# Kernel optimization log

Hardware: AMD Instinct MI355X
Metric: run time of the kernel (lower is better)

Reference implementation:

```python
import jax, jax.numpy as jnp
import numpy as np

E, N, D, H = 500000, 100000, 8, 256
BN_EPS = 1e-5


def _batchnorm(x, gamma, beta):
    # BatchNorm1d in training mode: biased batch statistics over dim 0
    mu = jnp.mean(x, axis=0)
    var = jnp.var(x, axis=0)
    return (x - mu) * jax.lax.rsqrt(var + BN_EPS) * gamma + beta


def _encoder(x, W1, b1, gamma, beta, W2, b2):
    h = jax.nn.relu(x @ W1 + b1)
    h = _batchnorm(h, gamma, beta)
    return h @ W2 + b2


def setup_inputs() -> dict:
    key = jax.random.key(0)
    ks = jax.random.split(key, 24)
    s = 0.05  # weight init scale
    inp = {
        "edge_attr": jax.random.normal(ks[0], (E, D), dtype=jnp.float32),
        "node_features": jax.random.normal(ks[1], (N, D), dtype=jnp.float32),
        "edge_index": jax.random.randint(ks[2], (2, E), 0, N, dtype=jnp.int32),
        "e_W1": jax.random.normal(ks[3], (D, H)) * s,
        "e_b1": jax.random.normal(ks[4], (H,)) * s,
        "e_gamma": jnp.ones((H,), jnp.float32),
        "e_beta": jnp.zeros((H,), jnp.float32),
        "e_W2": jax.random.normal(ks[5], (H, H)) * s,
        "e_b2": jax.random.normal(ks[6], (H,)) * s,
        "n_W1": jax.random.normal(ks[7], (D, H)) * s,
        "n_b1": jax.random.normal(ks[8], (H,)) * s,
        "n_gamma": jnp.ones((H,), jnp.float32),
        "n_beta": jnp.zeros((H,), jnp.float32),
        "n_W2": jax.random.normal(ks[9], (H, H)) * s,
        "n_b2": jax.random.normal(ks[10], (H,)) * s,
        "Wv": jax.random.normal(ks[11], (H, H)) * s,
        "bv": jax.random.normal(ks[12], (H,)) * s,
        "Wo": jax.random.normal(ks[13], (H, H)) * s,
        "bo": jax.random.normal(ks[14], (H,)) * s,
        "Wp": jax.random.normal(ks[15], (H, D)) * s,
        "bp": jax.random.normal(ks[16], (D,)) * s,
    }
    return inp


def reference(edge_attr, node_features, edge_index,
              e_W1, e_b1, e_gamma, e_beta, e_W2, e_b2,
              n_W1, n_b1, n_gamma, n_beta, n_W2, n_b2,
              Wv, bv, Wo, bo, Wp, bp):
    # edge encoder: Linear -> ReLU -> BatchNorm1d -> Linear
    edge_encoded = _encoder(edge_attr, e_W1, e_b1, e_gamma, e_beta, e_W2, e_b2)

    # gather endpoint features and average (node dim == edge dim, slice is no-op)
    src = node_features[edge_index[0]]  # [E, D]
    tgt = node_features[edge_index[1]]  # [E, D]
    node_context = (src + tgt) * 0.5
    node_encoded = _encoder(node_context, n_W1, n_b1, n_gamma, n_beta, n_W2, n_b2)

    # MultiheadAttention with seq_len=1: softmax over one key is exactly 1,
    # so output = out_proj(v_proj(node_encoded)); q/k projections cancel.
    attn_out = (node_encoded @ Wv + bv) @ Wo + bo  # [E, H]

    edge_attr_enhanced = attn_out @ Wp + bp  # [E, D]
    return edge_attr + 0.5 * edge_attr_enhanced
```

## Files before the change

### kernel.cpp

```cpp
#include <hip/hip_runtime.h>
#include <hip/hip_bf16.h>
#include <string.h>

#define E_CNT 500000
#define N_CNT 100000
#define HID   256
#define NTILE 31250

typedef short short8 __attribute__((ext_vector_type(8)));
typedef float f32x4 __attribute__((ext_vector_type(4)));

__device__ __forceinline__ unsigned short f2bf(float f){
  union { float f; unsigned int i; } v; v.f = f;
  unsigned int u = v.i;
  u = u + 0x7FFFu + ((u >> 16) & 1u);
  return (unsigned short)(u >> 16);
}

__device__ __forceinline__ unsigned int pk_bf16(float a, float b){
  __hip_bfloat162 p = __float22bfloat162_rn(make_float2(a, b));
  unsigned int u; memcpy(&u, &p, 4); return u;
}

__device__ __forceinline__ void init_w1_lds(unsigned short* w1l,
                                            const float* W1, const float* b1,
                                            int tid){
  int ch = tid;
  #pragma unroll
  for (int j = 0; j < 8; ++j){
    unsigned short w = f2bf(W1[j * HID + ch]);
    w1l[ch * 24 + j]     = w;
    w1l[ch * 24 + 8 + j] = w;
  }
  w1l[ch * 24 + 16] = f2bf(2.0f * b1[ch]);
  #pragma unroll
  for (int j = 17; j < 24; ++j) w1l[ch * 24 + j] = 0;
  if (tid < 32) w1l[256 * 24 + tid] = 0;
}

__global__ __launch_bounds__(256, 3) void k1_stats(
    const int* __restrict__ eidx, const float* __restrict__ nf,
    const float* __restrict__ W1, const float* __restrict__ b1,
    float* __restrict__ part, float* __restrict__ bd2,
    unsigned short* __restrict__ ctxw)
{
  __shared__ unsigned short w1l[256 * 24 + 32];
  __shared__ unsigned short ctx[4][16 * 40];
  __shared__ float sred[2][4][128];

  const int tid = threadIdx.x, lane = tid & 63, wid = tid >> 6;
  const int cg = wid & 1;
  const int pair = (blockIdx.x * 4 + wid) >> 1;
  const int npair = gridDim.x * 2;
  const int m = lane & 15, q = lane >> 4;
  const int r = lane >> 2, side = (lane >> 1) & 1, half = lane & 1;

  if (blockIdx.x == 0 && tid < 16) bd2[tid] = 0.f;

  init_w1_lds(w1l, W1, b1, tid);

  unsigned short* myctx = ctx[wid];
  for (int i = lane; i < 16 * 40; i += 64) myctx[i] = 0;
  if (lane < 16) myctx[lane * 40 + 16] = 0x3F80;
  __syncthreads();

  short8 w1fr[8];
  #pragma unroll
  for (int nt = 0; nt < 8; ++nt)
    w1fr[nt] = *(const short8*)&w1l[((cg * 8 + nt) * 16 + m) * 24 + q * 8];

  const f32x4 z4 = {0.f, 0.f, 0.f, 0.f};
  f32x4 sacc[8], qacc[8];
  #pragma unroll
  for (int nt = 0; nt < 8; ++nt){ sacc[nt] = z4; qacc[nt] = z4; }

  int t = pair;
  float4 nfc = make_float4(0.f,0.f,0.f,0.f); int i1 = 0;
  if (t < NTILE){
    int id0 = eidx[side * E_CNT + t * 16 + r];
    nfc = ((const float4*)nf)[id0 * 2 + half];
  }
  { int tn = t + npair;
    if (tn < NTILE) i1 = eidx[side * E_CNT + tn * 16 + r]; }

  for (; t < NTILE; t += npair){
    uint2 pkd = make_uint2(pk_bf16(nfc.x, nfc.y), pk_bf16(nfc.z, nfc.w));
    *(uint2*)&myctx[r * 40 + side * 8 + half * 4] = pkd;
    if (cg == 0)
      *(uint2*)&ctxw[(size_t)t * 256 + r * 16 + side * 8 + half * 4] = pkd;

    int tn1 = t + npair, tn2 = t + 2 * npair;
    float4 nfn = make_float4(0.f,0.f,0.f,0.f); int i2 = 0;
    if (tn1 < NTILE) nfn = ((const float4*)nf)[i1 * 2 + half];
    if (tn2 < NTILE) i2 = eidx[side * E_CNT + tn2 * 16 + r];

    asm volatile("s_waitcnt lgkmcnt(0)" ::: "memory");
    short8 bfr = *(const short8*)&myctx[m * 40 + q * 8];
    #pragma unroll
    for (int nt = 0; nt < 8; ++nt){
      f32x4 c = __builtin_amdgcn_mfma_f32_16x16x32_bf16(w1fr[nt], bfr, z4, 0, 0, 0);
      f32x4 hv = __builtin_elementwise_max(c, z4);
      sacc[nt] += hv;
      qacc[nt] += hv * hv;
    }
    nfc = nfn; i1 = i2;
  }

  #pragma unroll
  for (int nt = 0; nt < 8; ++nt){
    #pragma unroll
    for (int i = 0; i < 4; ++i){
      float v = sacc[nt][i], w = qacc[nt][i];
      v += __shfl_xor(v, 1); w += __shfl_xor(w, 1);
      v += __shfl_xor(v, 2); w += __shfl_xor(w, 2);
      v += __shfl_xor(v, 4); w += __shfl_xor(w, 4);
      v += __shfl_xor(v, 8); w += __shfl_xor(w, 8);
      if (m == 0){
        int loc = nt * 16 + q * 4 + i;
        sred[0][wid][loc] = v;
        sred[1][wid][loc] = w;
      }
    }
  }
  __syncthreads();
  {
    int j = tid, hf = j >> 7, loc = j & 127;
    float s0 = sred[0][hf][loc] + sred[0][hf + 2][loc];
    float s1 = sred[1][hf][loc] + sred[1][hf + 2][loc];
    part[blockIdx.x * 512 + j]       = s0;
    part[blockIdx.x * 512 + 256 + j] = s1;
  }
}

__global__ __launch_bounds__(256) void kMid(
    const float* __restrict__ part, int nb,
    const float* __restrict__ gamma, const float* __restrict__ beta,
    const float* __restrict__ nW2,
    const float* __restrict__ Wv, const float* __restrict__ Wo,
    const float* __restrict__ Wp,
    const float* __restrict__ bv, const float* __restrict__ bo,
    const float* __restrict__ bp, const float* __restrict__ nb2,
    unsigned short* __restrict__ wd2t, float* __restrict__ bd2)
{
  __shared__ float WpL[2048];
  __shared__ float T1L[2048];
  __shared__ float T2L[2048];
  __shared__ float scr[2048];
  __shared__ float stL[8];
  const int t = threadIdx.x, b = blockIdx.x;

  for (int i = t; i < 2048; i += 256) WpL[i] = Wp[i];
  __syncthreads();

  {
    const float4* row = (const float4*)(Wo + t * HID);
    f32x4 a0 = {0.f,0.f,0.f,0.f}, a1 = {0.f,0.f,0.f,0.f};
    #pragma unroll 8
    for (int j4 = 0; j4 < 64; ++j4){
      float4 w = row[j4];
      const f32x4* xp = (const f32x4*)&WpL[j4 * 32];
      a0 += w.x * xp[0]; a1 += w.x * xp[1];
      a0 += w.y * xp[2]; a1 += w.y * xp[3];
      a0 += w.z * xp[4]; a1 += w.z * xp[5];
      a0 += w.w * xp[6]; a1 += w.w * xp[7];
    }
    *(f32x4*)&T1L[t * 8]     = a0;
    *(f32x4*)&T1L[t * 8 + 4] = a1;
  }
  __syncthreads();

  {
    const float4* row = (const float4*)(Wv + t * HID);
    f32x4 a0 = {0.f,0.f,0.f,0.f}, a1 = {0.f,0.f,0.f,0.f};
    #pragma unroll 8
    for (int j4 = 0; j4 < 64; ++j4){
      float4 w = row[j4];
      const f32x4* xp = (const f32x4*)&T1L[j4 * 32];
      a0 += w.x * xp[0]; a1 += w.x * xp[1];
      a0 += w.y * xp[2]; a1 += w.y * xp[3];
      a0 += w.z * xp[4]; a1 += w.z * xp[5];
      a0 += w.w * xp[6]; a1 += w.w * xp[7];
    }
    *(f32x4*)&T2L[t * 8]     = a0;
    *(f32x4*)&T2L[t * 8 + 4] = a1;
  }
  __syncthreads();

  {
    int cl = t >> 6, i = t & 63;
    int c = b * 4 + cl;
    float s0 = 0.f, s1 = 0.f;
    for (int b2 = i; b2 < nb; b2 += 64){
      s0 += part[b2 * 512 + c];
      s1 += part[b2 * 512 + 256 + c];
    }
    scr[cl * 128 + i]      = s0;
    scr[cl * 128 + 64 + i] = s1;
  }
  __syncthreads();
  if (t < 4){
    float s0 = 0.f, s1 = 0.f;
    for (int i = 0; i < 64; ++i){
      s0 += scr[t * 128 + i];
      s1 += scr[t * 128 + 64 + i];
    }
    const float invE = 1.0f / (float)E_CNT;
    float mu  = s0 * invE;
    float var = fmaxf(s1 * invE - mu * mu, 0.f);
    float s   = gamma[b * 4 + t] * rsqrtf(var + 4.0f * 1e-5f);
    stL[t]     = s;
    stL[4 + t] = beta[b * 4 + t] - mu * s;
  }
  __syncthreads();

  {
    int cl = t >> 6, d = (t >> 3) & 7, p8 = t & 7;
    int c = b * 4 + cl;
    const float* row = nW2 + c * HID;
    float a = 0.f;
    for (int j = p8 * 32; j < p8 * 32 + 32; ++j)
      a = fmaf(row[j], T2L[j * 8 + d], a);
    scr[t] = a;
  }
  __syncthreads();
  {
    int cl = t >> 6, d = (t >> 3) & 7, p8 = t & 7;
    if (p8 == 0){
      float w = 0.f;
      #pragma unroll
      for (int i = 0; i < 8; ++i) w += scr[t + i];
      int c = b * 4 + cl;
      wd2t[d * HID + c]       = f2bf(0.5f * stL[cl] * w);
      wd2t[(8 + d) * HID + c] = 0;
      scr[1024 + cl * 8 + d]  = stL[4 + cl] * w;
    }
  }
  __syncthreads();
  if (t < 8){
    float a = scr[1024 + t] + scr[1024 + 8 + t] +
              scr[1024 + 16 + t] + scr[1024 + 24 + t];
    #pragma unroll
    for (int jj = 0; jj < 4; ++jj){
      int j = 4 * b + jj;
      a = fmaf(nb2[j], T2L[j * 8 + t], a);
      a = fmaf(bv[j],  T1L[j * 8 + t], a);
      a = fmaf(bo[j],  WpL[j * 8 + t], a);
    }
    if (b == 0) a += bp[t];
    atomicAdd(&bd2[t], a);
  }
}

__global__ __launch_bounds__(256, 3) void k3_main(
    const float* __restrict__ ea,
    const float* __restrict__ W1, const float* __restrict__ b1,
    const unsigned short* __restrict__ wd2t, const float* __restrict__ bd2,
    const unsigned short* __restrict__ ctxw,
    float* __restrict__ out)
{
  __shared__ __align__(16) unsigned short smem[4 * 16 * 264];

  const int tid = threadIdx.x, lane = tid & 63, wid = tid >> 6;
  const int gw = blockIdx.x * 4 + wid, ngw = gridDim.x * 4;
  const int m = lane & 15, q = lane >> 4;

  init_w1_lds(smem, W1, b1, tid);

  short8 w2fr[8];
  #pragma unroll
  for (int kb = 0; kb < 8; ++kb)
    w2fr[kb] = *(const short8*)&wd2t[m * HID + kb * 32 + q * 8];
  const float bd2v = (m < 8) ? 0.5f * bd2[m] : 0.f;

  __syncthreads();

  short8 w1fr[16];
  #pragma unroll
  for (int nt = 0; nt < 16; ++nt)
    w1fr[nt] = *(const short8*)&smem[(nt * 16 + m) * 24 + q * 8];

  __syncthreads();
  unsigned short* myh = smem + wid * (16 * 264);

  const f32x4 z4 = {0.f, 0.f, 0.f, 0.f};

  short8 kc = {0,0,0,0,0,0,0,0};
  if (q == 2) kc[0] = (short)0x3F80;
  const bool ld  = (q < 2);
  const bool dok = (m < 8);

  int t = gw;
  short8 bcur = kc;
  if (ld && t < NTILE)
    bcur = *(const short8*)&ctxw[(size_t)t * 256 + m * 16 + q * 8];

  for (; t < NTILE; t += ngw){
    int tn = t + ngw;
    short8 bnext = kc;
    if (ld && tn < NTILE)
      bnext = *(const short8*)&ctxw[(size_t)tn * 256 + m * 16 + q * 8];

    float eav[4];
    #pragma unroll
    for (int i = 0; i < 4; ++i)
      eav[i] = dok ? ea[(t * 16 + q * 4 + i) * 8 + m] : 0.f;

    #pragma unroll
    for (int nt = 0; nt < 16; ++nt){
      f32x4 c = __builtin_amdgcn_mfma_f32_16x16x32_bf16(w1fr[nt], bcur, z4, 0, 0, 0);
      f32x4 hv = __builtin_elementwise_max(c, z4);
      *(uint2*)&myh[m * 264 + nt * 16 + q * 4] =
          make_uint2(pk_bf16(hv[0], hv[1]), pk_bf16(hv[2], hv[3]));
    }
    asm volatile("s_waitcnt lgkmcnt(0)" ::: "memory");
    f32x4 acc0 = z4, acc1 = z4;
    #pragma unroll
    for (int kb = 0; kb < 4; ++kb){
      short8 a0 = *(const short8*)&myh[m * 264 + (2*kb)   * 32 + q * 8];
      short8 a1 = *(const short8*)&myh[m * 264 + (2*kb+1) * 32 + q * 8];
      acc0 = __builtin_amdgcn_mfma_f32_16x16x32_bf16(a0, w2fr[2*kb],   acc0, 0, 0, 0);
      acc1 = __builtin_amdgcn_mfma_f32_16x16x32_bf16(a1, w2fr[2*kb+1], acc1, 0, 0, 0);
    }
    if (dok){
      #pragma unroll
      for (int i = 0; i < 4; ++i){
        float o = eav[i] + acc0[i] + acc1[i] + bd2v;
        out[(t * 16 + q * 4 + i) * 8 + m] = o;
      }
    }
    bcur = bnext;
  }
}

extern "C" void kernel_launch(void* const* d_in, const int* in_sizes, int n_in,
                              void* d_out, int out_size, void* d_ws, size_t ws_size,
                              hipStream_t stream)
{
  const float* ea   = (const float*)d_in[0];
  const float* nf   = (const float*)d_in[1];
  const int*   eidx = (const int*)d_in[2];
  const float* nW1    = (const float*)d_in[9];
  const float* nb1    = (const float*)d_in[10];
  const float* ngamma = (const float*)d_in[11];
  const float* nbeta  = (const float*)d_in[12];
  const float* nW2    = (const float*)d_in[13];
  const float* nb2    = (const float*)d_in[14];
  const float* Wv     = (const float*)d_in[15];
  const float* bv     = (const float*)d_in[16];
  const float* Wo     = (const float*)d_in[17];
  const float* bo     = (const float*)d_in[18];
  const float* Wp     = (const float*)d_in[19];
  const float* bp     = (const float*)d_in[20];

  const size_t CTX_BYTES = (size_t)NTILE * 512;
  long avail = (long)ws_size - 8192 - 64 - (long)CTX_BYTES - 1024;
  int nb = (int)(avail / 2048);
  if (nb > 1792) nb = 1792;
  if (nb < 1)    nb = 1;

  char* ws = (char*)d_ws;
  size_t off = (size_t)nb * 2048;
  float* ws_part          = (float*)(ws + 0);
  unsigned short* ws_wd2t = (unsigned short*)(ws + off);
  float* ws_bd2           = (float*)(ws + off + 8192);
  unsigned short* ws_ctx  = (unsigned short*)(ws + off + 8192 + 64);

  k1_stats<<<dim3(nb), dim3(256), 0, stream>>>(eidx, nf, nW1, nb1,
                                               ws_part, ws_bd2, ws_ctx);
  kMid<<<dim3(64), dim3(256), 0, stream>>>(
      ws_part, nb, ngamma, nbeta, nW2, Wv, Wo, Wp, bv, bo, bp, nb2,
      ws_wd2t, ws_bd2);
  k3_main<<<dim3(1024), dim3(256), 0, stream>>>(
      ea, nW1, nb1, ws_wd2t, ws_bd2, ws_ctx, (float*)d_out);
}
```

Before: 213.8 us.

## Build MFMA B-fragments directly in registers and drop LDS context staging

The stats kernel now has each lane in quads 0-1 gather both halves of one endpoint's node features and pack them straight into the MFMA B operand in registers. This removes the per-wave LDS staging buffer and the lgkmcnt wait. The context workspace layout changes to a side-major [q*128 + m*8] order, and the main kernel's loads are updated to match. The stats kernel's grid cap is also reduced from 1792 to 1024 blocks, which trades parallelism for fewer partial sums to reduce. Half of the lanes now sit idle during gathers, and gather concurrency per wave changes.

Result: faster. 197.6 us (median of 2 runs) (-7.6%).

```diff
diff --git a/kernel.cpp b/kernel.cpp
--- a/kernel.cpp
+++ b/kernel.cpp
@@ -45,7 +45,6 @@
     unsigned short* __restrict__ ctxw)
 {
   __shared__ unsigned short w1l[256 * 24 + 32];
-  __shared__ unsigned short ctx[4][16 * 40];
   __shared__ float sred[2][4][128];
 
   const int tid = threadIdx.x, lane = tid & 63, wid = tid >> 6;
@@ -53,15 +52,10 @@
   const int pair = (blockIdx.x * 4 + wid) >> 1;
   const int npair = gridDim.x * 2;
   const int m = lane & 15, q = lane >> 4;
-  const int r = lane >> 2, side = (lane >> 1) & 1, half = lane & 1;
 
   if (blockIdx.x == 0 && tid < 16) bd2[tid] = 0.f;
 
   init_w1_lds(w1l, W1, b1, tid);
-
-  unsigned short* myctx = ctx[wid];
-  for (int i = lane; i < 16 * 40; i += 64) myctx[i] = 0;
-  if (lane < 16) myctx[lane * 40 + 16] = 0x3F80;
   __syncthreads();
 
   short8 w1fr[8];
@@ -74,28 +68,39 @@
   #pragma unroll
   for (int nt = 0; nt < 8; ++nt){ sacc[nt] = z4; qacc[nt] = z4; }
 
+  short8 kc = {0,0,0,0,0,0,0,0};
+  if (q == 2) kc[0] = (short)0x3F80;
+  const bool ld = (q < 2);
+
   int t = pair;
-  float4 nfc = make_float4(0.f,0.f,0.f,0.f); int i1 = 0;
-  if (t < NTILE){
-    int id0 = eidx[side * E_CNT + t * 16 + r];
-    nfc = ((const float4*)nf)[id0 * 2 + half];
-  }
-  { int tn = t + npair;
-    if (tn < NTILE) i1 = eidx[side * E_CNT + tn * 16 + r]; }
+  int idc = 0;
+  float4 nfa = make_float4(0.f,0.f,0.f,0.f), nfb = nfa;
+  if (ld){
+    int id0 = eidx[q * E_CNT + t * 16 + m];
+    nfa = ((const float4*)nf)[id0 * 2];
+    nfb = ((const float4*)nf)[id0 * 2 + 1];
+    int tn = t + npair;
+    if (tn < NTILE) idc = eidx[q * E_CNT + tn * 16 + m];
+  }
 
   for (; t < NTILE; t += npair){
-    uint2 pkd = make_uint2(pk_bf16(nfc.x, nfc.y), pk_bf16(nfc.z, nfc.w));
-    *(uint2*)&myctx[r * 40 + side * 8 + half * 4] = pkd;
-    if (cg == 0)
-      *(uint2*)&ctxw[(size_t)t * 256 + r * 16 + side * 8 + half * 4] = pkd;
+    short8 bfr = kc;
+    if (ld){
+      union { short8 s; uint4 u; } bu;
+      bu.u = make_uint4(pk_bf16(nfa.x, nfa.y), pk_bf16(nfa.z, nfa.w),
+                        pk_bf16(nfb.x, nfb.y), pk_bf16(nfb.z, nfb.w));
+      bfr = bu.s;
+      if (cg == 0)
+        *(uint4*)&ctxw[(size_t)t * 256 + q * 128 + m * 8] = bu.u;
+    }
 
     int tn1 = t + npair, tn2 = t + 2 * npair;
-    float4 nfn = make_float4(0.f,0.f,0.f,0.f); int i2 = 0;
-    if (tn1 < NTILE) nfn = ((const float4*)nf)[i1 * 2 + half];
-    if (tn2 < NTILE) i2 = eidx[side * E_CNT + tn2 * 16 + r];
-
-    asm volatile("s_waitcnt lgkmcnt(0)" ::: "memory");
-    short8 bfr = *(const short8*)&myctx[m * 40 + q * 8];
+    if (ld && tn1 < NTILE){
+      nfa = ((const float4*)nf)[idc * 2];
+      nfb = ((const float4*)nf)[idc * 2 + 1];
+      if (tn2 < NTILE) idc = eidx[q * E_CNT + tn2 * 16 + m];
+    }
+
     #pragma unroll
     for (int nt = 0; nt < 8; ++nt){
       f32x4 c = __builtin_amdgcn_mfma_f32_16x16x32_bf16(w1fr[nt], bfr, z4, 0, 0, 0);
@@ -103,7 +108,6 @@
       sacc[nt] += hv;
       qacc[nt] += hv * hv;
     }
-    nfc = nfn; i1 = i2;
   }
 
   #pragma unroll
@@ -292,13 +296,13 @@
   int t = gw;
   short8 bcur = kc;
   if (ld && t < NTILE)
-    bcur = *(const short8*)&ctxw[(size_t)t * 256 + m * 16 + q * 8];
+    bcur = *(const short8*)&ctxw[(size_t)t * 256 + q * 128 + m * 8];
 
   for (; t < NTILE; t += ngw){
     int tn = t + ngw;
     short8 bnext = kc;
     if (ld && tn < NTILE)
-      bnext = *(const short8*)&ctxw[(size_t)tn * 256 + m * 16 + q * 8];
+      bnext = *(const short8*)&ctxw[(size_t)tn * 256 + q * 128 + m * 8];
 
     float eav[4];
     #pragma unroll
@@ -355,7 +359,7 @@
   const size_t CTX_BYTES = (size_t)NTILE * 512;
   long avail = (long)ws_size - 8192 - 64 - (long)CTX_BYTES - 1024;
   int nb = (int)(avail / 2048);
-  if (nb > 1792) nb = 1792;
+  if (nb > 1024) nb = 1024;
   if (nb < 1)    nb = 1;
 
   char* ws = (char*)d_ws;
```
